# Optimization experiments

Measured on AMD Instinct MI355X. Metric: run time of the kernel, lower is better.

## Reference

```python
import jax, jax.numpy as jnp
import numpy as np

EPS = 1e-5

def _layernorm(x, g, b):
    mu = jnp.mean(x, axis=-1, keepdims=True)
    var = jnp.mean(jnp.square(x - mu), axis=-1, keepdims=True)
    return (x - mu) * jax.lax.rsqrt(var + EPS) * g + b

def _silu(x):
    return x * jax.nn.sigmoid(x)

def _xavier(key, shape):
    fan_out, fan_in = shape
    limit = np.sqrt(6.0 / (fan_in + fan_out))
    return jax.random.uniform(key, shape, jnp.float32, -limit, limit)

def setup_inputs() -> dict:
    key = jax.random.key(0)
    ks = jax.random.split(key, 4)
    B = 2097152
    return {
        'x': jax.random.normal(ks[0], (B, 24), jnp.float32),
        'w1': _xavier(ks[1], (64, 24)), 'b1': jnp.zeros((64,), jnp.float32),
        'g1': jnp.ones((64,), jnp.float32), 'be1': jnp.zeros((64,), jnp.float32),
        'w2': _xavier(ks[2], (64, 64)), 'b2': jnp.zeros((64,), jnp.float32),
        'g2': jnp.ones((64,), jnp.float32), 'be2': jnp.zeros((64,), jnp.float32),
        'w3': _xavier(ks[3], (7, 64)), 'b3': jnp.zeros((7,), jnp.float32),
        'g3': jnp.ones((7,), jnp.float32), 'be3': jnp.zeros((7,), jnp.float32),
    }

def reference(x, w1, b1, g1, be1, w2, b2, g2, be2, w3, b3, g3, be3):
    h = _silu(_layernorm(x @ w1.T + b1, g1, be1))      # [B, 64]
    h = _silu(_layernorm(h @ w2.T + b2, g2, be2))      # [B, 64]
    h = _layernorm(h @ w3.T + b3, g3, be3)             # [B, 7]
    return jax.nn.softmax(h, axis=-1)
```

## Files before the change

kernel.cpp:

```cpp
#include <hip/hip_runtime.h>
#include <math.h>

#define BLOCK 256
#define WPB 4
#define NBLOCKS 2048

typedef float  f32x4 __attribute__((ext_vector_type(4)));
typedef float  f32x2 __attribute__((ext_vector_type(2)));
typedef short  short8 __attribute__((ext_vector_type(8)));
typedef unsigned int u32;
typedef u32 u32x4 __attribute__((ext_vector_type(4)));
typedef u32 u32x2 __attribute__((ext_vector_type(2)));

static __device__ __forceinline__ f32x4 mfma16(short8 a, short8 b, f32x4 c) {
    return __builtin_amdgcn_mfma_f32_16x16x32_bf16(a, b, c, 0, 0, 0);
}

static __device__ __forceinline__ f32x4 zero4() { f32x4 z = {0.f, 0.f, 0.f, 0.f}; return z; }

static __device__ __forceinline__ u32 cvt_pk(float lo, float hi) {
    u32 r;
    asm("v_cvt_pk_bf16_f32 %0, %1, %2" : "=v"(r) : "v"(lo), "v"(hi));
    return r;
}
static __device__ __forceinline__ float unpk_lo(u32 p) { return __builtin_bit_cast(float, p << 16); }
static __device__ __forceinline__ float unpk_hi(u32 p) { return __builtin_bit_cast(float, p & 0xffff0000u); }

static __device__ __forceinline__ short8 mk_frag(u32 a, u32 b, u32 c, u32 d) {
    u32x4 t = {a, b, c, d};
    return __builtin_bit_cast(short8, t);
}

struct Frag2 { short8 hi, lo; };

static __device__ __forceinline__ Frag2 split8(f32x4 a, f32x4 b) {
    u32 h0 = cvt_pk(a[0], a[1]), h1 = cvt_pk(a[2], a[3]);
    u32 h2 = cvt_pk(b[0], b[1]), h3 = cvt_pk(b[2], b[3]);
    u32 l0 = cvt_pk(a[0] - unpk_lo(h0), a[1] - unpk_hi(h0));
    u32 l1 = cvt_pk(a[2] - unpk_lo(h1), a[3] - unpk_hi(h1));
    u32 l2 = cvt_pk(b[0] - unpk_lo(h2), b[1] - unpk_hi(h2));
    u32 l3 = cvt_pk(b[2] - unpk_lo(h3), b[3] - unpk_hi(h3));
    Frag2 r; r.hi = mk_frag(h0, h1, h2, h3); r.lo = mk_frag(l0, l1, l2, l3);
    return r;
}

static __device__ __forceinline__ void split4(f32x4 v, u32x2& hi, u32x2& lo) {
    u32 h0 = cvt_pk(v[0], v[1]), h1 = cvt_pk(v[2], v[3]);
    u32 l0 = cvt_pk(v[0] - unpk_lo(h0), v[1] - unpk_hi(h0));
    u32 l1 = cvt_pk(v[2] - unpk_lo(h1), v[3] - unpk_hi(h1));
    hi = u32x2{h0, h1}; lo = u32x2{l0, l1};
}

static __device__ __forceinline__ Frag2 wfrag(const float* p) {
    return split8(*(const f32x4*)p, *(const f32x4*)(p + 4));
}

static __device__ __forceinline__ float red4(float v) {
    v += __shfl_xor(v, 16);
    v += __shfl_xor(v, 32);
    return v;
}
static __device__ __forceinline__ float redmax4(float v) {
    v = fmaxf(v, __shfl_xor(v, 16));
    v = fmaxf(v, __shfl_xor(v, 32));
    return v;
}

struct TState {
    f32x4 xa, xb;
    f32x4 d[4];
    short8 bhHi[2], bhLo[2];
    f32x4 d3;
};

static __device__ __forceinline__ void ph_l1(TState& t, const Frag2& bx, const Frag2* w1f) {
#pragma unroll
    for (int mt = 0; mt < 4; ++mt) {
        f32x4 d = mfma16(w1f[mt].hi, bx.hi, zero4());
        d = mfma16(w1f[mt].hi, bx.lo, d);
        d = mfma16(w1f[mt].lo, bx.hi, d);
        t.d[mt] = d;
    }
}

static __device__ __forceinline__ void ph_l2_pair(TState& A, TState& B,
        const unsigned char* sW2h, const unsigned char* sW2l, u32 crow, u32 ch, int q) {
    const u32 r0 = crow + ((((u32)q) ^ ch) << 4);
    const u32 r1 = crow + ((((u32)(4 + q)) ^ ch) << 4);
#pragma unroll
    for (int mt = 0; mt < 4; ++mt) {
        const u32 mo = (u32)mt * 2048u;
        short8 h0 = *(const short8*)(sW2h + mo + r0);
        short8 h1 = *(const short8*)(sW2h + mo + r1);
        short8 l0 = *(const short8*)(sW2l + mo + r0);
        short8 l1 = *(const short8*)(sW2l + mo + r1);
        f32x4 d = mfma16(h0, A.bhHi[0], zero4());
        d = mfma16(h0, A.bhLo[0], d);
        d = mfma16(l0, A.bhHi[0], d);
        d = mfma16(h1, A.bhHi[1], d);
        d = mfma16(h1, A.bhLo[1], d);
        d = mfma16(l1, A.bhHi[1], d);
        A.d[mt] = d;
        f32x4 e = mfma16(h0, B.bhHi[0], zero4());
        e = mfma16(h0, B.bhLo[0], e);
        e = mfma16(l0, B.bhHi[0], e);
        e = mfma16(h1, B.bhHi[1], e);
        e = mfma16(h1, B.bhLo[1], e);
        e = mfma16(l1, B.bhHi[1], e);
        B.d[mt] = e;
    }
}

static __device__ __forceinline__ void ph_l3(TState& t, const Frag2* w3f) {
    f32x4 a = mfma16(w3f[0].hi, t.bhHi[0], zero4());
    a = mfma16(w3f[0].hi, t.bhLo[0], a);
    a = mfma16(w3f[0].lo, t.bhHi[0], a);
    f32x4 b = mfma16(w3f[1].hi, t.bhHi[1], zero4());
    b = mfma16(w3f[1].hi, t.bhLo[1], b);
    b = mfma16(w3f[1].lo, t.bhHi[1], b);
#pragma unroll
    for (int r = 0; r < 4; ++r) t.d3[r] = a[r] + b[r];
}

template<int PB, int PG, int PBE>
static __device__ __forceinline__ void ph_ln_silu(TState& t, const float* sP, int q) {
    float s = 0.f, s2 = 0.f;
#pragma unroll
    for (int mt = 0; mt < 4; ++mt) {
        if (PB >= 0) {
            const f32x4 bv = *(const f32x4*)(sP + PB + mt * 16 + q * 4);
#pragma unroll
            for (int r = 0; r < 4; ++r) t.d[mt][r] += bv[r];
        }
#pragma unroll
        for (int r = 0; r < 4; ++r) { float v = t.d[mt][r]; s += v; s2 = fmaf(v, v, s2); }
    }
    s = red4(s); s2 = red4(s2);
    const float mu = s * (1.f / 64.f);
    const float var = s2 * (1.f / 64.f) - mu * mu;
    const float inv = __builtin_amdgcn_rsqf(var + 1e-5f);
    const float cns = -mu * inv;
#pragma unroll
    for (int mt = 0; mt < 4; ++mt) {
        const f32x4 gv  = *(const f32x4*)(sP + PG  + mt * 16 + q * 4);
        const f32x4 bev = *(const f32x4*)(sP + PBE + mt * 16 + q * 4);
#pragma unroll
        for (int r = 0; r < 4; ++r) {
            float tt = fmaf(t.d[mt][r], inv, cns);
            float v  = fmaf(tt, gv[r], bev[r]);
            t.d[mt][r] = v * __builtin_amdgcn_rcpf(1.f + __expf(-v));
        }
    }
}

static __device__ __forceinline__ void ph_stage(TState& t, unsigned char* sHi, unsigned char* sLo,
                                                u32 crow, u32 ch, int q) {
#pragma unroll
    for (int mt = 0; mt < 4; ++mt) {
        u32x2 hi, lo;
        split4(t.d[mt], hi, lo);
        u32 off = crow + ((((u32)(mt * 2 + (q >> 1))) ^ ch) << 4) + (u32)((q & 1) * 8);
        *(u32x2*)(sHi + off) = hi;
        *(u32x2*)(sLo + off) = lo;
    }
#pragma unroll
    for (int kk = 0; kk < 2; ++kk) {
        u32 roff = crow + ((((u32)(kk * 4 + q)) ^ ch) << 4);
        t.bhHi[kk] = *(const short8*)(sHi + roff);
        t.bhLo[kk] = *(const short8*)(sLo + roff);
    }
}

static __device__ __forceinline__ void ph_out(TState& t, const float* sP, int q, int c, int lane,
                                              unsigned char* ob, float* out, int tile, bool valid,
                                              int oc0, int of0, int oc1, int of1) {
    const f32x4 b3v  = *(const f32x4*)(sP + 384 + q * 4);
    const f32x4 g3v  = *(const f32x4*)(sP + 400 + q * 4);
    const f32x4 be3v = *(const f32x4*)(sP + 416 + q * 4);
    f32x4 d3 = t.d3;
    float s = 0.f, s2 = 0.f;
#pragma unroll
    for (int r = 0; r < 4; ++r) {
        float v = d3[r] + b3v[r];
        d3[r] = v;
        const bool ok = (q * 4 + r) < 7;
        if (ok) { s += v; s2 = fmaf(v, v, s2); }
    }
    s = red4(s); s2 = red4(s2);
    const float mu = s * (1.f / 7.f);
    const float var = s2 * (1.f / 7.f) - mu * mu;
    const float inv = __builtin_amdgcn_rsqf(var + 1e-5f);
    const float cns = -mu * inv;

    float z[4]; float mx = -1e30f;
#pragma unroll
    for (int r = 0; r < 4; ++r) {
        z[r] = fmaf(fmaf(d3[r], inv, cns), g3v[r], be3v[r]);
        const bool ok = (q * 4 + r) < 7;
        if (ok) mx = fmaxf(mx, z[r]);
    }
    mx = redmax4(mx);
    float es = 0.f; float e[4];
#pragma unroll
    for (int r = 0; r < 4; ++r) {
        const bool ok = (q * 4 + r) < 7;
        e[r] = ok ? __expf(z[r] - mx) : 0.f;
        es += e[r];
    }
    es = red4(es);
    const float rs = __builtin_amdgcn_rcpf(es);

    if (q == 0) {
        f32x4 v = {e[0] * rs, e[1] * rs, e[2] * rs, e[3] * rs};
        *(f32x4*)(ob + c * 48) = v;
    } else if (q == 1) {
        f32x2 v = {e[0] * rs, e[1] * rs};
        *(f32x2*)(ob + c * 48 + 16) = v;
        *(float*)(ob + c * 48 + 24) = e[2] * rs;
    }
    if (valid) {
        float* outp = out + (size_t)tile * 112;
        outp[lane] = *(const float*)(ob + oc0 * 48 + of0 * 4);
        if (lane < 48) outp[64 + lane] = *(const float*)(ob + oc1 * 48 + of1 * 4);
    }
}

__global__ __launch_bounds__(BLOCK, 3) void mlp_mfma3_kernel(
    const float* __restrict__ x,
    const float* __restrict__ w1, const float* __restrict__ b1,
    const float* __restrict__ g1, const float* __restrict__ be1,
    const float* __restrict__ w2, const float* __restrict__ b2,
    const float* __restrict__ g2, const float* __restrict__ be2,
    const float* __restrict__ w3, const float* __restrict__ b3,
    const float* __restrict__ g3, const float* __restrict__ be3,
    float* __restrict__ out, int ntiles)
{
    __shared__ __align__(16) unsigned char smem[WPB * 8192 + 16384];
    __shared__ __align__(16) float sP[6 * 64 + 3 * 16];

    const int tid = threadIdx.x;
    const int lane = tid & 63;
    const int wib  = tid >> 6;
    const int c = lane & 15;
    const int q = lane >> 4;

    unsigned char* wb   = smem + wib * 8192;
    unsigned char* sHiA = wb;
    unsigned char* sLoA = wb + 2048;
    unsigned char* sHiB = wb + 4096;
    unsigned char* sLoB = wb + 6144;
    unsigned char* obA  = sHiA;
    unsigned char* obB  = sHiB;
    unsigned char* sW2h = smem + WPB * 8192;
    unsigned char* sW2l = sW2h + 8192;

    for (int i = tid; i < 512; i += BLOCK) {
        const int row = i >> 3, cb = i & 7;
        Frag2 f = wfrag(w2 + row * 64 + cb * 8);
        const u32 off = (u32)row * 128u + (u32)((cb ^ (row & 7)) << 4);
        *(short8*)(sW2h + off) = f.hi;
        *(short8*)(sW2l + off) = f.lo;
    }
    if (tid < 64) {
        sP[        tid] = b1[tid];  sP[ 64 + tid] = g1[tid];  sP[128 + tid] = be1[tid];
        sP[192 + tid] = b2[tid];    sP[256 + tid] = g2[tid];  sP[320 + tid] = be2[tid];
    }
    if (tid < 16) {
        const bool ok = tid < 7;
        sP[384 + tid] = ok ? b3[tid]  : 0.f;
        sP[400 + tid] = ok ? g3[tid]  : 0.f;
        sP[416 + tid] = ok ? be3[tid] : 0.f;
    }

    const u32 crow = (u32)c * 128u;
    const u32 ch   = (u32)(c & 7);

    Frag2 w1f[4];
#pragma unroll
    for (int mt = 0; mt < 4; ++mt) {
        if (q < 3) {
            w1f[mt] = wfrag(w1 + (mt * 16 + c) * 24 + q * 8);
        } else {
            float s = b1[mt * 16 + c];
            f32x4 a = {s, 0.f, 0.f, 0.f};
            w1f[mt] = split8(a, zero4());
        }
    }
    Frag2 w3f[2];
#pragma unroll
    for (int kk = 0; kk < 2; ++kk) {
        if (c < 7) w3f[kk] = wfrag(w3 + c * 64 + kk * 32 + q * 8);
        else       { w3f[kk].hi = mk_frag(0,0,0,0); w3f[kk].lo = mk_frag(0,0,0,0); }
    }

    __syncthreads();

    const int oc0 = lane / 7, of0 = lane - oc0 * 7;
    const int i1 = lane + 64;
    const int oc1 = i1 / 7, of1 = i1 - oc1 * 7;

    const int wid = blockIdx.x * WPB + wib;
    const int ts  = gridDim.x * WPB;

    TState A, B;
    A.xa = zero4(); A.xb = zero4(); B.xa = zero4(); B.xb = zero4();
    {
        const int t0 = wid, t1 = wid + ts;
        if (t0 < ntiles && q < 3) {
            const float* xp = x + ((size_t)t0 * 16 + c) * 24 + q * 8;
            A.xa = *(const f32x4*)xp; A.xb = *(const f32x4*)(xp + 4);
        }
        if (t1 < ntiles && q < 3) {
            const float* xp = x + ((size_t)t1 * 16 + c) * 24 + q * 8;
            B.xa = *(const f32x4*)xp; B.xb = *(const f32x4*)(xp + 4);
        }
        if (q == 3) { A.xa[0] = 1.0f; B.xa[0] = 1.0f; }
    }

    for (int tile = wid; tile < ntiles; tile += 2 * ts) {
        asm volatile("" ::: "memory");

        const int tB = tile + ts;
        const bool vB = tB < ntiles;

        Frag2 bxA = split8(A.xa, A.xb);
        Frag2 bxB = split8(B.xa, B.xb);

        {
            const int tA2 = tile + 2 * ts, tB2 = tile + 3 * ts;
            if (tA2 < ntiles && q < 3) {
                const float* xp = x + ((size_t)tA2 * 16 + c) * 24 + q * 8;
                A.xa = *(const f32x4*)xp; A.xb = *(const f32x4*)(xp + 4);
            }
            if (tB2 < ntiles && q < 3) {
                const float* xp = x + ((size_t)tB2 * 16 + c) * 24 + q * 8;
                B.xa = *(const f32x4*)xp; B.xb = *(const f32x4*)(xp + 4);
            }
        }

        ph_l1(A, bxA, w1f);                 ph_l1(B, bxB, w1f);
        ph_ln_silu<-1, 64, 128>(A, sP, q);  ph_ln_silu<-1, 64, 128>(B, sP, q);
        ph_stage(A, sHiA, sLoA, crow, ch, q); ph_stage(B, sHiB, sLoB, crow, ch, q);
        ph_l2_pair(A, B, sW2h, sW2l, crow, ch, q);
        ph_ln_silu<192, 256, 320>(A, sP, q); ph_ln_silu<192, 256, 320>(B, sP, q);
        ph_stage(A, sHiA, sLoA, crow, ch, q); ph_stage(B, sHiB, sLoB, crow, ch, q);
        ph_l3(A, w3f);                      ph_l3(B, w3f);
        ph_out(A, sP, q, c, lane, obA, out, tile, true, oc0, of0, oc1, of1);
        ph_out(B, sP, q, c, lane, obB, out, tB,   vB,   oc0, of0, oc1, of1);
    }
}

extern "C" void kernel_launch(void* const* d_in, const int* in_sizes, int n_in,
                              void* d_out, int out_size, void* d_ws, size_t ws_size,
                              hipStream_t stream) {
    const float* x   = (const float*)d_in[0];
    const float* w1  = (const float*)d_in[1];
    const float* b1  = (const float*)d_in[2];
    const float* g1  = (const float*)d_in[3];
    const float* be1 = (const float*)d_in[4];
    const float* w2  = (const float*)d_in[5];
    const float* b2  = (const float*)d_in[6];
    const float* g2  = (const float*)d_in[7];
    const float* be2 = (const float*)d_in[8];
    const float* w3  = (const float*)d_in[9];
    const float* b3  = (const float*)d_in[10];
    const float* g3  = (const float*)d_in[11];
    const float* be3 = (const float*)d_in[12];
    float* out = (float*)d_out;

    const int B = in_sizes[0] / 24;
    const int ntiles = B / 16;
    hipLaunchKernelGGL(mlp_mfma3_kernel, dim3(NBLOCKS), dim3(BLOCK), 0, stream,
                       x, w1, b1, g1, be1, w2, b2, g2, be2, w3, b3, g3, be3,
                       out, ntiles);
}
```

Baseline: 224.5 us.

## Process one tile per wave iteration instead of interleaving two tiles

Removes the two-tile (A/B) interleaving in the main loop, so each wave handles a single 16-row tile per iteration with one-tile-ahead prefetch of x. This halves the per-wave LDS staging buffer and cuts register pressure, which could allow higher occupancy. In exchange it loses the instruction-level parallelism and the W2 fragment reuse across two tiles, so LDS reads of W2 per tile double and MFMA chains are less overlapped.

```diff
diff --git a/kernel.cpp b/kernel.cpp
--- a/kernel.cpp
+++ b/kernel.cpp
@@ -83,7 +83,7 @@
     }
 }
 
-static __device__ __forceinline__ void ph_l2_pair(TState& A, TState& B,
+static __device__ __forceinline__ void ph_l2_lds(TState& t,
         const unsigned char* sW2h, const unsigned char* sW2l, u32 crow, u32 ch, int q) {
     const u32 r0 = crow + ((((u32)q) ^ ch) << 4);
     const u32 r1 = crow + ((((u32)(4 + q)) ^ ch) << 4);
@@ -94,20 +94,13 @@
         short8 h1 = *(const short8*)(sW2h + mo + r1);
         short8 l0 = *(const short8*)(sW2l + mo + r0);
         short8 l1 = *(const short8*)(sW2l + mo + r1);
-        f32x4 d = mfma16(h0, A.bhHi[0], zero4());
-        d = mfma16(h0, A.bhLo[0], d);
-        d = mfma16(l0, A.bhHi[0], d);
-        d = mfma16(h1, A.bhHi[1], d);
-        d = mfma16(h1, A.bhLo[1], d);
-        d = mfma16(l1, A.bhHi[1], d);
-        A.d[mt] = d;
-        f32x4 e = mfma16(h0, B.bhHi[0], zero4());
-        e = mfma16(h0, B.bhLo[0], e);
-        e = mfma16(l0, B.bhHi[0], e);
-        e = mfma16(h1, B.bhHi[1], e);
-        e = mfma16(h1, B.bhLo[1], e);
-        e = mfma16(l1, B.bhHi[1], e);
-        B.d[mt] = e;
+        f32x4 d = mfma16(h0, t.bhHi[0], zero4());
+        d = mfma16(h0, t.bhLo[0], d);
+        d = mfma16(l0, t.bhHi[0], d);
+        d = mfma16(h1, t.bhHi[1], d);
+        d = mfma16(h1, t.bhLo[1], d);
+        d = mfma16(l1, t.bhHi[1], d);
+        t.d[mt] = d;
     }
 }
 
@@ -172,7 +165,7 @@
 }
 
 static __device__ __forceinline__ void ph_out(TState& t, const float* sP, int q, int c, int lane,
-                                              unsigned char* ob, float* out, int tile, bool valid,
+                                              unsigned char* ob, float* out, int tile,
                                               int oc0, int of0, int oc1, int of1) {
     const f32x4 b3v  = *(const f32x4*)(sP + 384 + q * 4);
     const f32x4 g3v  = *(const f32x4*)(sP + 400 + q * 4);
@@ -218,14 +211,12 @@
         *(f32x2*)(ob + c * 48 + 16) = v;
         *(float*)(ob + c * 48 + 24) = e[2] * rs;
     }
-    if (valid) {
-        float* outp = out + (size_t)tile * 112;
-        outp[lane] = *(const float*)(ob + oc0 * 48 + of0 * 4);
-        if (lane < 48) outp[64 + lane] = *(const float*)(ob + oc1 * 48 + of1 * 4);
-    }
-}
-
-__global__ __launch_bounds__(BLOCK, 3) void mlp_mfma3_kernel(
+    float* outp = out + (size_t)tile * 112;
+    outp[lane] = *(const float*)(ob + oc0 * 48 + of0 * 4);
+    if (lane < 48) outp[64 + lane] = *(const float*)(ob + oc1 * 48 + of1 * 4);
+}
+
+__global__ __launch_bounds__(BLOCK, 3) void mlp_mfma4_kernel(
     const float* __restrict__ x,
     const float* __restrict__ w1, const float* __restrict__ b1,
     const float* __restrict__ g1, const float* __restrict__ be1,
@@ -235,7 +226,7 @@
     const float* __restrict__ g3, const float* __restrict__ be3,
     float* __restrict__ out, int ntiles)
 {
-    __shared__ __align__(16) unsigned char smem[WPB * 8192 + 16384];
+    __shared__ __align__(16) unsigned char smem[WPB * 4096 + 16384];
     __shared__ __align__(16) float sP[6 * 64 + 3 * 16];
 
     const int tid = threadIdx.x;
@@ -244,14 +235,11 @@
     const int c = lane & 15;
     const int q = lane >> 4;
 
-    unsigned char* wb   = smem + wib * 8192;
-    unsigned char* sHiA = wb;
-    unsigned char* sLoA = wb + 2048;
-    unsigned char* sHiB = wb + 4096;
-    unsigned char* sLoB = wb + 6144;
-    unsigned char* obA  = sHiA;
-    unsigned char* obB  = sHiB;
-    unsigned char* sW2h = smem + WPB * 8192;
+    unsigned char* wb   = smem + wib * 4096;
+    unsigned char* sHi  = wb;
+    unsigned char* sLo  = wb + 2048;
+    unsigned char* ob   = sHi;
+    unsigned char* sW2h = smem + WPB * 4096;
     unsigned char* sW2l = sW2h + 8192;
 
     for (int i = tid; i < 512; i += BLOCK) {
@@ -302,51 +290,35 @@
     const int wid = blockIdx.x * WPB + wib;
     const int ts  = gridDim.x * WPB;
 
-    TState A, B;
-    A.xa = zero4(); A.xb = zero4(); B.xa = zero4(); B.xb = zero4();
-    {
-        const int t0 = wid, t1 = wid + ts;
-        if (t0 < ntiles && q < 3) {
-            const float* xp = x + ((size_t)t0 * 16 + c) * 24 + q * 8;
-            A.xa = *(const f32x4*)xp; A.xb = *(const f32x4*)(xp + 4);
-        }
-        if (t1 < ntiles && q < 3) {
-            const float* xp = x + ((size_t)t1 * 16 + c) * 24 + q * 8;
-            B.xa = *(const f32x4*)xp; B.xb = *(const f32x4*)(xp + 4);
-        }
-        if (q == 3) { A.xa[0] = 1.0f; B.xa[0] = 1.0f; }
-    }
-
-    for (int tile = wid; tile < ntiles; tile += 2 * ts) {
+    TState A;
+    A.xa = zero4(); A.xb = zero4();
+    if (wid < ntiles && q < 3) {
+        const float* xp = x + ((size_t)wid * 16 + c) * 24 + q * 8;
+        A.xa = *(const f32x4*)xp; A.xb = *(const f32x4*)(xp + 4);
+    }
+    if (q == 3) A.xa[0] = 1.0f;
+
+    for (int tile = wid; tile < ntiles; tile += ts) {
         asm volatile("" ::: "memory");
 
-        const int tB = tile + ts;
-        const bool vB = tB < ntiles;
-
-        Frag2 bxA = split8(A.xa, A.xb);
-        Frag2 bxB = split8(B.xa, B.xb);
+        Frag2 bx = split8(A.xa, A.xb);
 
         {
-            const int tA2 = tile + 2 * ts, tB2 = tile + 3 * ts;
-            if (tA2 < ntiles && q < 3) {
-                const float* xp = x + ((size_t)tA2 * 16 + c) * 24 + q * 8;
+            const int nt = tile + ts;
+            if (nt < ntiles && q < 3) {
+                const float* xp = x + ((size_t)nt * 16 + c) * 24 + q * 8;
                 A.xa = *(const f32x4*)xp; A.xb = *(const f32x4*)(xp + 4);
             }
-            if (tB2 < ntiles && q < 3) {
-                const float* xp = x + ((size_t)tB2 * 16 + c) * 24 + q * 8;
-                B.xa = *(const f32x4*)xp; B.xb = *(const f32x4*)(xp + 4);
-            }
         }
 
-        ph_l1(A, bxA, w1f);                 ph_l1(B, bxB, w1f);
-        ph_ln_silu<-1, 64, 128>(A, sP, q);  ph_ln_silu<-1, 64, 128>(B, sP, q);
-        ph_stage(A, sHiA, sLoA, crow, ch, q); ph_stage(B, sHiB, sLoB, crow, ch, q);
-        ph_l2_pair(A, B, sW2h, sW2l, crow, ch, q);
-        ph_ln_silu<192, 256, 320>(A, sP, q); ph_ln_silu<192, 256, 320>(B, sP, q);
-        ph_stage(A, sHiA, sLoA, crow, ch, q); ph_stage(B, sHiB, sLoB, crow, ch, q);
-        ph_l3(A, w3f);                      ph_l3(B, w3f);
-        ph_out(A, sP, q, c, lane, obA, out, tile, true, oc0, of0, oc1, of1);
-        ph_out(B, sP, q, c, lane, obB, out, tB,   vB,   oc0, of0, oc1, of1);
+        ph_l1(A, bx, w1f);
+        ph_ln_silu<-1, 64, 128>(A, sP, q);
+        ph_stage(A, sHi, sLo, crow, ch, q);
+        ph_l2_lds(A, sW2h, sW2l, crow, ch, q);
+        ph_ln_silu<192, 256, 320>(A, sP, q);
+        ph_stage(A, sHi, sLo, crow, ch, q);
+        ph_l3(A, w3f);
+        ph_out(A, sP, q, c, lane, ob, out, tile, oc0, of0, oc1, of1);
     }
 }
 
@@ -370,7 +342,7 @@
 
     const int B = in_sizes[0] / 24;
     const int ntiles = B / 16;
-    hipLaunchKernelGGL(mlp_mfma3_kernel, dim3(NBLOCKS), dim3(BLOCK), 0, stream,
+    hipLaunchKernelGGL(mlp_mfma4_kernel, dim3(NBLOCKS), dim3(BLOCK), 0, stream,
                        x, w1, b1, g1, be1, w2, b2, g2, be2, w3, b3, g3, be3,
                        out, ntiles);
 }
```

Measured after the change: 190.0 us. 15.4% less time.
